# Optimization experiments

Measured on AMD Instinct MI355X. Metric: run time of the kernel, lower is better.

The kernel has to match this reference:

```python
import jax, jax.numpy as jnp
import numpy as np
from jax import lax

# Per-tensor power-of-two scales (ScalingImplType.CONST / POWER_OF_TWO in Brevitas)
S_ACT8 = 2.0 ** -4   # 8-bit signed input quant scale
S_ACT4 = 2.0 ** -1   # 4-bit signed input quant scale
S_W = 2.0 ** -2      # per-tensor weight quant scale
S_RELU = 2.0 ** -2   # 4-bit unsigned QuantReLU scale


def fq(x, scale, qmin, qmax):
    # fake-quant with straight-through estimator (STE)
    q = jnp.clip(jnp.round(x / scale), qmin, qmax) * scale
    return x + lax.stop_gradient(q - x)


def fq_signed(x, scale, bits):
    return fq(x, scale, -(2 ** (bits - 1)), 2 ** (bits - 1) - 1)


def fq_uint(x, scale, bits):
    return fq(x, scale, 0, 2 ** bits - 1)


def qconv(x, w, in_bits, w_bits, s_in, stride=1, padding=0, groups=1):
    xq = fq_signed(x, s_in, in_bits)
    wq = fq_signed(w, S_W, w_bits)
    return lax.conv_general_dilated(
        xq, wq, (stride, stride), [(padding, padding)] * 2,
        feature_group_count=groups,
        dimension_numbers=('NCHW', 'OIHW', 'NCHW'))


def maxpool(x, k, s):
    return lax.reduce_window(x, -jnp.inf, lax.max,
                             (1, 1, k, k), (1, 1, s, s), 'VALID')


def dwsep(x, dw, pw):
    c = x.shape[1]
    x = qconv(x, dw, 4, 4, S_ACT4, padding=1, groups=c)  # depthwise 3x3
    x = qconv(x, pw, 4, 4, S_ACT4)                       # pointwise 1x1
    return x


def qrelu4(x):
    return fq_uint(jax.nn.relu(x), S_RELU, 4)


def setup_inputs() -> dict:
    key = jax.random.key(0)
    ks = jax.random.split(key, 10)
    B = 1024
    mk = lambda k, shp, sc=0.5: jax.random.normal(k, shp, jnp.float32) * sc
    return {
        'x': jax.random.normal(ks[0], (B, 3, 32, 32), jnp.float32),
        'w0': mk(ks[1], (3, 3, 1, 1)),
        'dw1': mk(ks[2], (3, 1, 3, 3)),
        'pw1': mk(ks[3], (32, 3, 1, 1)),
        'dw2': mk(ks[4], (32, 1, 3, 3)),
        'pw2': mk(ks[5], (64, 32, 1, 1)),
        'dw3': mk(ks[6], (64, 1, 3, 3)),
        'pw3': mk(ks[7], (128, 64, 1, 1)),
        'wc1': mk(ks[8], (256, 128, 1, 1)),
        'wc2': mk(ks[9], (10, 256, 1, 1)),
    }


def reference(x, w0, dw1, pw1, dw2, pw2, dw3, pw3, wc1, wc2):
    # features
    h = qconv(x, w0, 8, 8, S_ACT8)            # 1x1, 3->3, 8-bit
    h = dwsep(h, dw1, pw1)                    # 3->32, 32x32
    h = qrelu4(h)
    h = maxpool(h, 2, 2)                      # 16x16
    h = dwsep(h, dw2, pw2)                    # 32->64
    h = qrelu4(h)
    h = maxpool(h, 2, 2)                      # 8x8
    h = dwsep(h, dw3, pw3)                    # 64->128
    h = qrelu4(h)
    h = maxpool(h, 8, 1)                      # 1x1
    # classifier
    h = qconv(h, wc1, 4, 4, S_ACT4)           # 128->256
    h = qrelu4(h)
    h = qconv(h, wc2, 4, 4, S_ACT4)           # 256->10
    h = fq_signed(h, S_ACT8, 8)               # output quant int8
    return h
```

## Files before the change

kernel.cpp:

```cpp
#include <hip/hip_runtime.h>

typedef int v4i __attribute__((ext_vector_type(4)));

#define W0i   0
#define DW1i  9
#define PW1i  36
#define DW2i  132
#define WC1p  3556
#define WC2p  11748
#define PW2Fb 12388
#define PW3Fb 12900
#define DW2pk 14948
#define DW3pk 15092
#define WTOT  15380

__device__ __forceinline__ int iclamp(int v, int lo, int hi) {
  return v < lo ? lo : (v > hi ? hi : v);
}
__device__ __forceinline__ int rne4(int a) {
  return (a + 1 + ((a >> 2) & 1)) >> 2;
}
__device__ __forceinline__ int rne32(int a) {
  return (a + 15 + ((a >> 5) & 1)) >> 5;
}

__device__ __forceinline__ void bar_lds() {
  asm volatile("s_waitcnt lgkmcnt(0)\n\ts_barrier" ::: "memory");
}

__device__ __forceinline__ int dot4(int a, int b, int c) {
#if defined(__has_builtin) && __has_builtin(__builtin_amdgcn_sdot4)
  return __builtin_amdgcn_sdot4(a, b, c, false);
#else
  c += ((a << 24) >> 24) * ((b << 24) >> 24);
  c += ((a << 16) >> 24) * ((b << 16) >> 24);
  c += ((a <<  8) >> 24) * ((b <<  8) >> 24);
  c += (a >> 24) * (b >> 24);
  return c;
#endif
}

__device__ __forceinline__ int alignb(int hi, int lo, int sh) {
#if defined(__has_builtin) && __has_builtin(__builtin_amdgcn_alignbyte)
  return __builtin_amdgcn_alignbyte(hi, lo, sh);
#else
  return (int)(((((unsigned long long)(unsigned)hi) << 32) |
                (unsigned)lo) >> (8 * sh));
#endif
}

__device__ __forceinline__ int pack3(int a, int b, int c) {
  return (a & 0xff) | ((b & 0xff) << 8) | ((c & 0xff) << 16);
}

__device__ __forceinline__ int pk_mad16(int a, int b, int c) {
  int d;
  asm("v_pk_mad_i16 %0, %1, %2, %3" : "=v"(d) : "v"(a), "v"(b), "v"(c));
  return d;
}
__device__ __forceinline__ int pk_add16(int a, int b) {
  int d;
  asm("v_pk_add_i16 %0, %1, %2" : "=v"(d) : "v"(a), "v"(b));
  return d;
}
__device__ __forceinline__ int pk_ashr16(int sh, int a) {
  int d;
  asm("v_pk_ashrrev_i16 %0, %1, %2" : "=v"(d) : "v"(sh), "v"(a));
  return d;
}
__device__ __forceinline__ int pk_max16(int a, int b) {
  int d;
  asm("v_pk_max_i16 %0, %1, %2" : "=v"(d) : "v"(a), "v"(b));
  return d;
}
__device__ __forceinline__ int pk_min16(int a, int b) {
  int d;
  asm("v_pk_min_i16 %0, %1, %2" : "=v"(d) : "v"(a), "v"(b));
  return d;
}
__device__ __forceinline__ int rne4s_pk(int a) {
  const int sh = 0x00020002, one = 0x00010001;
  int t = pk_ashr16(sh, a);
  t &= one;
  t += one;
  int s4 = pk_add16(a, t);
  int r = pk_ashr16(sh, s4);
  r = pk_max16(r, (int)0xFFF8FFF8);
  r = pk_min16(r, 0x00070007);
  return r;
}

__device__ __forceinline__ int max4(v4i d) {
  int a = d[0] > d[1] ? d[0] : d[1];
  int b = d[2] > d[3] ? d[2] : d[3];
  return a > b ? a : b;
}

__global__ __launch_bounds__(256) void prep_weights(
    const float* __restrict__ w0,  const float* __restrict__ dw1,
    const float* __restrict__ pw1, const float* __restrict__ dw2,
    const float* __restrict__ pw2, const float* __restrict__ dw3,
    const float* __restrict__ pw3, const float* __restrict__ wc1,
    const float* __restrict__ wc2, int* __restrict__ ws) {
  int t = blockIdx.x * blockDim.x + threadIdx.x;
  if (t >= WTOT) return;
  if (t >= DW2i && t < WC1p) return;
  if (t < DW2i) {
    float w; int lo = -8, hi = 7;
    if (t < DW1i)      { w = w0[t];        lo = -128; hi = 127; }
    else if (t < PW1i)   w = dw1[t - DW1i];
    else                 w = pw1[t - PW1i];
    ws[t] = iclamp((int)rintf(w * 4.f), lo, hi);
  } else if (t < PW2Fb) {
    const float* src = (t < WC2p) ? wc1 + (t - WC1p) * 4
                                  : wc2 + (t - WC2p) * 4;
    int p = 0;
#pragma unroll
    for (int b = 0; b < 4; b++) {
      int c = iclamp((int)rintf(src[b] * 4.f), -8, 7);
      p |= (c & 0xff) << (8 * b);
    }
    ws[t] = p;
  } else if (t < PW3Fb) {
    int i = t - PW2Fb;
    int nt = i >> 7, r = i & 127, lane = r >> 1, dw = r & 1;
    int n = nt * 16 + (lane & 15);
    int kb = (lane >> 4) * 8 + dw * 4;
    int p = 0;
#pragma unroll
    for (int b = 0; b < 4; b++) {
      int c = iclamp((int)rintf(pw2[n * 32 + kb + b] * 4.f), -8, 7);
      p |= (c & 0xff) << (8 * b);
    }
    ws[t] = p;
  } else if (t < DW2pk) {
    int i = t - PW3Fb;
    int g = i >> 7, r = i & 127, lane = r >> 1, dw = r & 1;
    int nt = g >> 1, kh = g & 1;
    int n = nt * 16 + (lane & 15);
    int kb = kh * 32 + (lane >> 4) * 8 + dw * 4;
    int p = 0;
#pragma unroll
    for (int b = 0; b < 4; b++) {
      int c = iclamp((int)rintf(pw3[n * 64 + kb + b] * 4.f), -8, 7);
      p |= (c & 0xff) << (8 * b);
    }
    ws[t] = p;
  } else if (t < DW3pk) {
    int i = t - DW2pk;
    int cq = i / 18, r = i - cq * 18, t9 = r >> 1, par = r & 1;
    int wl = iclamp((int)rintf(dw2[(cq * 4 + par) * 9 + t9] * 4.f), -8, 7);
    int wh = iclamp((int)rintf(dw2[(cq * 4 + 2 + par) * 9 + t9] * 4.f), -8, 7);
    ws[t] = (wl & 0xFFFF) | (wh << 16);
  } else {
    int i = t - DW3pk;
    int cq = i / 18, r = i - cq * 18, t9 = r >> 1, par = r & 1;
    int wl = iclamp((int)rintf(dw3[(cq * 4 + par) * 9 + t9] * 4.f), -8, 7);
    int wh = iclamp((int)rintf(dw3[(cq * 4 + 2 + par) * 9 + t9] * 4.f), -8, 7);
    ws[t] = (wl & 0xFFFF) | (wh << 16);
  }
}

__global__ __launch_bounds__(256, 4) void fused_net(
    const float* __restrict__ x,
    const int*   __restrict__ wq,
    float* __restrict__ out)
{
  const int img = blockIdx.x;
  const int tid = threadIdx.x;
  const int wv = tid >> 6, lane = tid & 63;
  const int lm = lane & 15, kg = lane >> 4;

  __shared__ __align__(16) int bufAi[2560];
  __shared__ __align__(16) int bufBi[2592];

  const int ntp = (wv & 1) * 2;
  const long bw0 = *(const long*)(wq + PW2Fb + (ntp * 64 + lane) * 2);
  const long bw1 = *(const long*)(wq + PW2Fb + ((ntp + 1) * 64 + lane) * 2);
  long b0v[2], b1v[2];
#pragma unroll
  for (int h = 0; h < 2; h++) {
    int nt = wv * 2 + h;
    b0v[h] = *(const long*)(wq + PW3Fb + (nt * 2 + 0) * 128 + lane * 2);
    b1v[h] = *(const long*)(wq + PW3Fb + (nt * 2 + 1) * 128 + lane * 2);
  }

  {
    const float* xim = x + (size_t)img * 3072;
    const int p4 = tid * 4;
    float4 v0 = *(const float4*)(xim + p4);
    float4 v1 = *(const float4*)(xim + 1024 + p4);
    float4 v2 = *(const float4*)(xim + 2048 + p4);
    int w[9];
#pragma unroll
    for (int i = 0; i < 9; i++) w[i] = wq[W0i + i];
#define Q8(v) iclamp((int)rintf((v) * 16.f), -128, 127)
    int a0[4] = {Q8(v0.x), Q8(v0.y), Q8(v0.z), Q8(v0.w)};
    int a1[4] = {Q8(v1.x), Q8(v1.y), Q8(v1.z), Q8(v1.w)};
    int a2[4] = {Q8(v2.x), Q8(v2.y), Q8(v2.z), Q8(v2.w)};
#undef Q8
#pragma unroll
    for (int o = 0; o < 3; o++) {
      int pk = 0;
#pragma unroll
      for (int j = 0; j < 4; j++) {
        int s = a0[j] * w[o * 3] + a1[j] * w[o * 3 + 1] + a2[j] * w[o * 3 + 2];
        pk |= (iclamp(rne32(s), -8, 7) & 0xff) << (8 * j);
      }
      bufAi[o * 256 + tid] = pk;
    }
  }
  bar_lds();

  {
    const int py = tid >> 4, px = tid & 15;
    int wr[3][3], wrh[3][3];
#pragma unroll
    for (int c = 0; c < 3; c++)
#pragma unroll
      for (int ky = 0; ky < 3; ky++) {
        int w = pack3(wq[DW1i + c * 9 + ky * 3],
                      wq[DW1i + c * 9 + ky * 3 + 1],
                      wq[DW1i + c * 9 + ky * 3 + 2]);
        wr[c][ky] = w;
        wrh[c][ky] = w << 8;
      }
    const int s = (px & 1) ? 1 : 3;
    const int D0 = (2 * px - 1) >> 2;
    int V[3][4];
#pragma unroll
    for (int r = 0; r < 4; r++) {
      int rr = 2 * py - 1 + r;
      bool ok = (unsigned)rr < 32u;
#pragma unroll
      for (int c = 0; c < 3; c++) {
        int lo = 0, hi = 0;
        if (ok) {
          const int* ap = bufAi + c * 256 + rr * 8;
          if (px > 0)  lo = ap[D0];
          if (px < 15) hi = ap[D0 + 1];
        }
        V[c][r] = alignb(hi, lo, s);
      }
    }
    int a[4];
#pragma unroll
    for (int dy = 0; dy < 2; dy++) {
      int r01[3];
#pragma unroll
      for (int c = 0; c < 3; c++) {
        int acc0 = 0, acc1 = 0;
#pragma unroll
        for (int ky = 0; ky < 3; ky++) {
          acc0 = dot4(V[c][dy + ky], wr[c][ky], acc0);
          acc1 = dot4(V[c][dy + ky], wrh[c][ky], acc1);
        }
        int p = (int)__builtin_amdgcn_perm((unsigned)acc1, (unsigned)acc0,
                                           0x05040100u);
        r01[c] = rne4s_pk(p);
      }
      unsigned t0 = __builtin_amdgcn_perm((unsigned)r01[1], (unsigned)r01[0],
                                          0x0C0C0400u);
      a[2 * dy] = (int)__builtin_amdgcn_perm((unsigned)r01[2], t0, 0x0C040100u);
      unsigned t1 = __builtin_amdgcn_perm((unsigned)r01[1], (unsigned)r01[0],
                                          0x0C0C0602u);
      a[2 * dy + 1] =
          (int)__builtin_amdgcn_perm((unsigned)r01[2], t1, 0x0C060100u);
    }
#pragma unroll
    for (int it = 0; it < 8; it++) {
      int pk = 0;
#pragma unroll
      for (int j = 0; j < 4; j++) {
        int o = it * 4 + j;
        int wpk = pack3(wq[PW1i + o * 3], wq[PW1i + o * 3 + 1],
                        wq[PW1i + o * 3 + 2]);
        int m0 = dot4(a[0], wpk, 0), m1 = dot4(a[1], wpk, 0);
        int m2 = dot4(a[2], wpk, 0), m3 = dot4(a[3], wpk, 0);
        int mx = max(max(m0, m1), max(m2, m3));
        pk |= iclamp(rne4(mx), 0, 7) << (8 * j);
      }
      bufBi[py * 149 + px * 9 + it] = pk;
    }
  }
  bar_lds();

  {
    const int cq = tid >> 5;
    const int rem = tid & 31;
    const int y = rem >> 1, xh = rem & 1, x0 = xh * 8;
    int we[9], wo[9];
    {
      const int2* wp = (const int2*)(wq + DW2pk + cq * 18);
#pragma unroll
      for (int t9 = 0; t9 < 9; t9++) { int2 v = wp[t9]; we[t9] = v.x; wo[t9] = v.y; }
    }
    int acce[8] = {}, acco[8] = {};
#pragma unroll
    for (int ky = 0; ky < 3; ky++) {
      int yy = y + ky - 1;
      if (yy < 0 || yy > 15) continue;
      int rb = yy * 149 + cq;
      int rd[10];
      rd[0] = (x0 > 0) ? bufBi[rb + (x0 - 1) * 9] : 0;
#pragma unroll
      for (int k = 1; k < 9; k++) rd[k] = bufBi[rb + (x0 - 1 + k) * 9];
      rd[9] = (x0 < 8) ? bufBi[rb + (x0 + 8) * 9] : 0;
      int ee[10], eo[10];
#pragma unroll
      for (int k = 0; k < 10; k++) {
        ee[k] = rd[k] & 0x000F000F;
        eo[k] = (rd[k] >> 8) & 0x000F000F;
      }
#pragma unroll
      for (int j = 0; j < 8; j++)
#pragma unroll
        for (int kx = 0; kx < 3; kx++) {
          acce[j] = pk_mad16(ee[j + kx], we[ky * 3 + kx], acce[j]);
          acco[j] = pk_mad16(eo[j + kx], wo[ky * 3 + kx], acco[j]);
        }
    }
    const int py = y >> 1, dy = y & 1;
#pragma unroll
    for (int j = 0; j < 8; j++) {
      int xx = x0 + j;
      int qp = py * 8 + (xx >> 1);
      int q = qp ^ (py & 3);
      int m = q * 4 + dy * 2 + (xx & 1);
      int re = rne4s_pk(acce[j]);
      int ro = rne4s_pk(acco[j]);
      bufAi[m * 10 + cq] = (re & 0x00FF00FF) | ((ro & 0x00FF00FF) << 8);
    }
  }
  bar_lds();

  {
    const int mtb = (wv >> 1) * 8;
    const signed char* Ab = (const signed char*)bufAi;
    signed char* A2c = (signed char*)bufBi;
    const int n0 = ntp * 16 + lm, n1 = (ntp + 1) * 16 + lm;
#pragma unroll 4
    for (int mt = mtb; mt < mtb + 8; mt++) {
      int m = mt * 16 + lm;
      long av = *(const long*)(Ab + m * 40 + kg * 8);
      v4i d0 = __builtin_amdgcn_mfma_i32_16x16x32_i8(av, bw0, (v4i){0, 0, 0, 0},
                                                     0, 0, 0);
      v4i d1 = __builtin_amdgcn_mfma_i32_16x16x32_i8(av, bw1, (v4i){0, 0, 0, 0},
                                                     0, 0, 0);
      int q = mt * 4 + kg;
      int qp = q ^ ((q >> 3) & 3);
      int py = qp >> 3, px = qp & 7;
      int bb = (py * 137 + px * 17) * 4;
      A2c[bb + n0] = (signed char)iclamp(rne4(max4(d0)), 0, 7);
      A2c[bb + n1] = (signed char)iclamp(rne4(max4(d1)), 0, 7);
    }
  }
  bar_lds();

  {
    int cq2 = tid >> 4;
    int s = tid & 15;
    int y = s >> 1, x0 = (s & 1) << 2;
    int we[9], wo[9];
    {
      const int2* wp = (const int2*)(wq + DW3pk + cq2 * 18);
#pragma unroll
      for (int t9 = 0; t9 < 9; t9++) { int2 v = wp[t9]; we[t9] = v.x; wo[t9] = v.y; }
    }
    int acce[4] = {}, acco[4] = {};
#pragma unroll
    for (int ky = 0; ky < 3; ky++) {
      int yy = y + ky - 1;
      if (yy < 0 || yy > 7) continue;
      int rb = yy * 137 + cq2;
      int rd[6];
      rd[0] = (x0 == 4) ? bufBi[rb + (x0 - 1) * 17] : 0;
      rd[1] = bufBi[rb + x0 * 17];
      rd[2] = bufBi[rb + (x0 + 1) * 17];
      rd[3] = bufBi[rb + (x0 + 2) * 17];
      rd[4] = bufBi[rb + (x0 + 3) * 17];
      rd[5] = (x0 == 0) ? bufBi[rb + (x0 + 4) * 17] : 0;
      int ee[6], eo[6];
#pragma unroll
      for (int k = 0; k < 6; k++) {
        ee[k] = rd[k] & 0x000F000F;
        eo[k] = (rd[k] >> 8) & 0x000F000F;
      }
#pragma unroll
      for (int j = 0; j < 4; j++)
#pragma unroll
        for (int kx = 0; kx < 3; kx++) {
          acce[j] = pk_mad16(ee[j + kx], we[ky * 3 + kx], acce[j]);
          acco[j] = pk_mad16(eo[j + kx], wo[ky * 3 + kx], acco[j]);
        }
    }
#pragma unroll
    for (int j = 0; j < 4; j++) {
      int re = rne4s_pk(acce[j]);
      int ro = rne4s_pk(acco[j]);
      bufAi[(y * 8 + x0 + j) * 18 + cq2] =
          (re & 0x00FF00FF) | ((ro & 0x00FF00FF) << 8);
    }
  }
  int4 wfc[8];
  {
    const int4* wp = (const int4*)(wq + WC1p + tid * 32);
#pragma unroll
    for (int rI = 0; rI < 8; rI++) wfc[rI] = wp[rI];
  }
  bar_lds();

  {
    const signed char* Ab = (const signed char*)bufAi;
    signed char* fcin = (signed char*)bufBi;
    int mx[2] = {-1000000, -1000000};
#pragma unroll
    for (int mt = 0; mt < 4; mt++) {
      int m = mt * 16 + lm;
      long a0 = *(const long*)(Ab + m * 72 + kg * 8);
      long a1 = *(const long*)(Ab + m * 72 + 32 + kg * 8);
#pragma unroll
      for (int h = 0; h < 2; h++) {
        v4i d = __builtin_amdgcn_mfma_i32_16x16x32_i8(a0, b0v[h],
                                                      (v4i){0, 0, 0, 0}, 0, 0, 0);
        d = __builtin_amdgcn_mfma_i32_16x16x32_i8(a1, b1v[h], d, 0, 0, 0);
        int t4 = max4(d);
        mx[h] = mx[h] > t4 ? mx[h] : t4;
      }
    }
#pragma unroll
    for (int h = 0; h < 2; h++) {
      int red = max(mx[h], __shfl_xor(mx[h], 16));
      red = max(red, __shfl_xor(red, 32));
      if (lane < 16)
        fcin[(wv * 2 + h) * 16 + lm] = (signed char)iclamp(rne4(red), 0, 7);
    }
  }
  bar_lds();

  {
    const int4* mp = (const int4*)bufBi;
    int acc = 0;
#pragma unroll
    for (int rI = 0; rI < 8; rI++) {
      int4 a = mp[rI]; int4 w = wfc[rI];
      acc = dot4(a.x, w.x, acc); acc = dot4(a.y, w.y, acc);
      acc = dot4(a.z, w.z, acc); acc = dot4(a.w, w.w, acc);
    }
    ((signed char*)bufAi)[tid] = (signed char)iclamp(rne4(acc), 0, 7);
  }
  bar_lds();

  if (tid < 40) {
    int k = tid >> 2, j = tid & 3;
    const int4* wp = (const int4*)(wq + WC2p + k * 64 + j * 16);
    const int4* ap = (const int4*)bufAi;
    int acc = 0;
#pragma unroll
    for (int r = 0; r < 4; r++) {
      int4 a = ap[j * 4 + r]; int4 w = wp[r];
      acc = dot4(a.x, w.x, acc); acc = dot4(a.y, w.y, acc);
      acc = dot4(a.z, w.z, acc); acc = dot4(a.w, w.w, acc);
    }
    acc += __shfl_xor(acc, 1);
    acc += __shfl_xor(acc, 2);
    if (j == 0) {
      int code = iclamp(2 * acc, -128, 127);
      out[(size_t)img * 10 + k] = (float)code * 0.0625f;
    }
  }
}

extern "C" void kernel_launch(void* const* d_in, const int* in_sizes, int n_in,
                              void* d_out, int out_size, void* d_ws, size_t ws_size,
                              hipStream_t stream) {
  const float* x   = (const float*)d_in[0];
  const float* w0  = (const float*)d_in[1];
  const float* dw1 = (const float*)d_in[2];
  const float* pw1 = (const float*)d_in[3];
  const float* dw2 = (const float*)d_in[4];
  const float* pw2 = (const float*)d_in[5];
  const float* dw3 = (const float*)d_in[6];
  const float* pw3 = (const float*)d_in[7];
  const float* wc1 = (const float*)d_in[8];
  const float* wc2 = (const float*)d_in[9];
  int*   wsq = (int*)d_ws;
  float* out = (float*)d_out;

  prep_weights<<<(WTOT + 255) / 256, 256, 0, stream>>>(
      w0, dw1, pw1, dw2, pw2, dw3, pw3, wc1, wc2, wsq);
  fused_net<<<1024, 256, 0, stream>>>(x, wsq, out);
}
```

Before: 93.06 us.

## Fold weight quantization into fused kernel and drop separate prep launch

Removes the prep_weights kernel and has every block quantize and pack the weights itself, straight from the float inputs. Small depthwise and pointwise weights are staged into shared memory, and MFMA and classifier weights are quantized in registers. This removes one kernel launch and the dependency between the two kernels. In exchange, each of the 1024 blocks re-reads the float weights, including 128 KB of wc1, and repeats the quantization arithmetic, which adds redundant global traffic and ALU work.

Measured after the change: 115.4 us. +24.1%, slower.

```diff
diff --git a/kernel.cpp b/kernel.cpp
--- a/kernel.cpp
+++ b/kernel.cpp
@@ -2,17 +2,12 @@
 
 typedef int v4i __attribute__((ext_vector_type(4)));
 
-#define W0i   0
-#define DW1i  9
-#define PW1i  36
-#define DW2i  132
-#define WC1p  3556
-#define WC2p  11748
-#define PW2Fb 12388
-#define PW3Fb 12900
-#define DW2pk 14948
-#define DW3pk 15092
-#define WTOT  15380
+#define W0s   0
+#define DW1s  9
+#define DW2s  18
+#define DW3s  162
+#define PW1s  452
+#define WSMN  484
 
 __device__ __forceinline__ int iclamp(int v, int lo, int hi) {
   return v < lo ? lo : (v > hi ? hi : v);
@@ -53,6 +48,20 @@
   return (a & 0xff) | ((b & 0xff) << 8) | ((c & 0xff) << 16);
 }
 
+__device__ __forceinline__ int q4w(float w) {
+  return iclamp((int)rintf(w * 4.f), -8, 7);
+}
+__device__ __forceinline__ int qpack4(const float* p) {
+  float4 v = *(const float4*)p;
+  return (q4w(v.x) & 0xff) | ((q4w(v.y) & 0xff) << 8) |
+         ((q4w(v.z) & 0xff) << 16) | (q4w(v.w) << 24);
+}
+__device__ __forceinline__ long qpack8(const float* p) {
+  unsigned lo = (unsigned)qpack4(p);
+  unsigned hi = (unsigned)qpack4(p + 4);
+  return (long)(((unsigned long long)hi << 32) | lo);
+}
+
 __device__ __forceinline__ int pk_mad16(int a, int b, int c) {
   int d;
   asm("v_pk_mad_i16 %0, %1, %2, %3" : "=v"(d) : "v"(a), "v"(b), "v"(c));
@@ -96,74 +105,13 @@
   return a > b ? a : b;
 }
 
-__global__ __launch_bounds__(256) void prep_weights(
-    const float* __restrict__ w0,  const float* __restrict__ dw1,
-    const float* __restrict__ pw1, const float* __restrict__ dw2,
-    const float* __restrict__ pw2, const float* __restrict__ dw3,
-    const float* __restrict__ pw3, const float* __restrict__ wc1,
-    const float* __restrict__ wc2, int* __restrict__ ws) {
-  int t = blockIdx.x * blockDim.x + threadIdx.x;
-  if (t >= WTOT) return;
-  if (t >= DW2i && t < WC1p) return;
-  if (t < DW2i) {
-    float w; int lo = -8, hi = 7;
-    if (t < DW1i)      { w = w0[t];        lo = -128; hi = 127; }
-    else if (t < PW1i)   w = dw1[t - DW1i];
-    else                 w = pw1[t - PW1i];
-    ws[t] = iclamp((int)rintf(w * 4.f), lo, hi);
-  } else if (t < PW2Fb) {
-    const float* src = (t < WC2p) ? wc1 + (t - WC1p) * 4
-                                  : wc2 + (t - WC2p) * 4;
-    int p = 0;
-#pragma unroll
-    for (int b = 0; b < 4; b++) {
-      int c = iclamp((int)rintf(src[b] * 4.f), -8, 7);
-      p |= (c & 0xff) << (8 * b);
-    }
-    ws[t] = p;
-  } else if (t < PW3Fb) {
-    int i = t - PW2Fb;
-    int nt = i >> 7, r = i & 127, lane = r >> 1, dw = r & 1;
-    int n = nt * 16 + (lane & 15);
-    int kb = (lane >> 4) * 8 + dw * 4;
-    int p = 0;
-#pragma unroll
-    for (int b = 0; b < 4; b++) {
-      int c = iclamp((int)rintf(pw2[n * 32 + kb + b] * 4.f), -8, 7);
-      p |= (c & 0xff) << (8 * b);
-    }
-    ws[t] = p;
-  } else if (t < DW2pk) {
-    int i = t - PW3Fb;
-    int g = i >> 7, r = i & 127, lane = r >> 1, dw = r & 1;
-    int nt = g >> 1, kh = g & 1;
-    int n = nt * 16 + (lane & 15);
-    int kb = kh * 32 + (lane >> 4) * 8 + dw * 4;
-    int p = 0;
-#pragma unroll
-    for (int b = 0; b < 4; b++) {
-      int c = iclamp((int)rintf(pw3[n * 64 + kb + b] * 4.f), -8, 7);
-      p |= (c & 0xff) << (8 * b);
-    }
-    ws[t] = p;
-  } else if (t < DW3pk) {
-    int i = t - DW2pk;
-    int cq = i / 18, r = i - cq * 18, t9 = r >> 1, par = r & 1;
-    int wl = iclamp((int)rintf(dw2[(cq * 4 + par) * 9 + t9] * 4.f), -8, 7);
-    int wh = iclamp((int)rintf(dw2[(cq * 4 + 2 + par) * 9 + t9] * 4.f), -8, 7);
-    ws[t] = (wl & 0xFFFF) | (wh << 16);
-  } else {
-    int i = t - DW3pk;
-    int cq = i / 18, r = i - cq * 18, t9 = r >> 1, par = r & 1;
-    int wl = iclamp((int)rintf(dw3[(cq * 4 + par) * 9 + t9] * 4.f), -8, 7);
-    int wh = iclamp((int)rintf(dw3[(cq * 4 + 2 + par) * 9 + t9] * 4.f), -8, 7);
-    ws[t] = (wl & 0xFFFF) | (wh << 16);
-  }
-}
-
 __global__ __launch_bounds__(256, 4) void fused_net(
     const float* __restrict__ x,
-    const int*   __restrict__ wq,
+    const float* __restrict__ w0f,  const float* __restrict__ dw1f,
+    const float* __restrict__ pw1f, const float* __restrict__ dw2f,
+    const float* __restrict__ pw2f, const float* __restrict__ dw3f,
+    const float* __restrict__ pw3f, const float* __restrict__ wc1f,
+    const float* __restrict__ wc2f,
     float* __restrict__ out)
 {
   const int img = blockIdx.x;
@@ -173,38 +121,73 @@
 
   __shared__ __align__(16) int bufAi[2560];
   __shared__ __align__(16) int bufBi[2592];
+  __shared__ __align__(16) int wsm[WSMN];
 
   const int ntp = (wv & 1) * 2;
-  const long bw0 = *(const long*)(wq + PW2Fb + (ntp * 64 + lane) * 2);
-  const long bw1 = *(const long*)(wq + PW2Fb + ((ntp + 1) * 64 + lane) * 2);
-  long b0v[2], b1v[2];
-#pragma unroll
-  for (int h = 0; h < 2; h++) {
-    int nt = wv * 2 + h;
-    b0v[h] = *(const long*)(wq + PW3Fb + (nt * 2 + 0) * 128 + lane * 2);
-    b1v[h] = *(const long*)(wq + PW3Fb + (nt * 2 + 1) * 128 + lane * 2);
-  }
-
-  {
-    const float* xim = x + (size_t)img * 3072;
-    const int p4 = tid * 4;
-    float4 v0 = *(const float4*)(xim + p4);
-    float4 v1 = *(const float4*)(xim + 1024 + p4);
-    float4 v2 = *(const float4*)(xim + 2048 + p4);
+  long bw0, bw1, b0v[2], b1v[2];
+  {
+    const int n0 = ntp * 16 + lm, n1 = (ntp + 1) * 16 + lm;
+    bw0 = qpack8(pw2f + n0 * 32 + kg * 8);
+    bw1 = qpack8(pw2f + n1 * 32 + kg * 8);
+#pragma unroll
+    for (int h = 0; h < 2; h++) {
+      int n = (wv * 2 + h) * 16 + lm;
+      b0v[h] = qpack8(pw3f + n * 64 + kg * 8);
+      b1v[h] = qpack8(pw3f + n * 64 + 32 + kg * 8);
+    }
+  }
+
+  for (int t = tid; t < WSMN; t += 256) {
+    int v;
+    if (t < 9) {
+      v = iclamp((int)rintf(w0f[t] * 4.f), -128, 127);
+    } else if (t < 18) {
+      int i = (t - 9) * 3;
+      v = pack3(q4w(dw1f[i]), q4w(dw1f[i + 1]), q4w(dw1f[i + 2]));
+    } else if (t < 162) {
+      int i = t - DW2s;
+      int cq = i / 18, r = i - cq * 18, t9 = r >> 1, par = r & 1;
+      int wl = q4w(dw2f[(cq * 4 + par) * 9 + t9]);
+      int wh = q4w(dw2f[(cq * 4 + 2 + par) * 9 + t9]);
+      v = (wl & 0xFFFF) | (wh << 16);
+    } else if (t < 450) {
+      int i = t - DW3s;
+      int cq = i / 18, r = i - cq * 18, t9 = r >> 1, par = r & 1;
+      int wl = q4w(dw3f[(cq * 4 + par) * 9 + t9]);
+      int wh = q4w(dw3f[(cq * 4 + 2 + par) * 9 + t9]);
+      v = (wl & 0xFFFF) | (wh << 16);
+    } else if (t >= PW1s) {
+      int o = (t - PW1s) * 3;
+      v = pack3(q4w(pw1f[o]), q4w(pw1f[o + 1]), q4w(pw1f[o + 2]));
+    } else {
+      continue;
+    }
+    wsm[t] = v;
+  }
+
+  const float* xim = x + (size_t)img * 3072;
+  const int p4 = tid * 4;
+  float4 v0 = *(const float4*)(xim + p4);
+  float4 v1 = *(const float4*)(xim + 1024 + p4);
+  float4 v2 = *(const float4*)(xim + 2048 + p4);
+#define Q8(v) iclamp((int)rintf((v) * 16.f), -128, 127)
+  int a0q[4] = {Q8(v0.x), Q8(v0.y), Q8(v0.z), Q8(v0.w)};
+  int a1q[4] = {Q8(v1.x), Q8(v1.y), Q8(v1.z), Q8(v1.w)};
+  int a2q[4] = {Q8(v2.x), Q8(v2.y), Q8(v2.z), Q8(v2.w)};
+#undef Q8
+  bar_lds();
+
+  {
     int w[9];
 #pragma unroll
-    for (int i = 0; i < 9; i++) w[i] = wq[W0i + i];
-#define Q8(v) iclamp((int)rintf((v) * 16.f), -128, 127)
-    int a0[4] = {Q8(v0.x), Q8(v0.y), Q8(v0.z), Q8(v0.w)};
-    int a1[4] = {Q8(v1.x), Q8(v1.y), Q8(v1.z), Q8(v1.w)};
-    int a2[4] = {Q8(v2.x), Q8(v2.y), Q8(v2.z), Q8(v2.w)};
-#undef Q8
+    for (int i = 0; i < 9; i++) w[i] = wsm[W0s + i];
 #pragma unroll
     for (int o = 0; o < 3; o++) {
       int pk = 0;
 #pragma unroll
       for (int j = 0; j < 4; j++) {
-        int s = a0[j] * w[o * 3] + a1[j] * w[o * 3 + 1] + a2[j] * w[o * 3 + 2];
+        int s = a0q[j] * w[o * 3] + a1q[j] * w[o * 3 + 1] +
+                a2q[j] * w[o * 3 + 2];
         pk |= (iclamp(rne32(s), -8, 7) & 0xff) << (8 * j);
       }
       bufAi[o * 256 + tid] = pk;
@@ -219,9 +202,7 @@
     for (int c = 0; c < 3; c++)
 #pragma unroll
       for (int ky = 0; ky < 3; ky++) {
-        int w = pack3(wq[DW1i + c * 9 + ky * 3],
-                      wq[DW1i + c * 9 + ky * 3 + 1],
-                      wq[DW1i + c * 9 + ky * 3 + 2]);
+        int w = wsm[DW1s + c * 3 + ky];
         wr[c][ky] = w;
         wrh[c][ky] = w << 8;
       }
@@ -273,8 +254,7 @@
 #pragma unroll
       for (int j = 0; j < 4; j++) {
         int o = it * 4 + j;
-        int wpk = pack3(wq[PW1i + o * 3], wq[PW1i + o * 3 + 1],
-                        wq[PW1i + o * 3 + 2]);
+        int wpk = wsm[PW1s + o];
         int m0 = dot4(a[0], wpk, 0), m1 = dot4(a[1], wpk, 0);
         int m2 = dot4(a[2], wpk, 0), m3 = dot4(a[3], wpk, 0);
         int mx = max(max(m0, m1), max(m2, m3));
@@ -291,7 +271,7 @@
     const int y = rem >> 1, xh = rem & 1, x0 = xh * 8;
     int we[9], wo[9];
     {
-      const int2* wp = (const int2*)(wq + DW2pk + cq * 18);
+      const int2* wp = (const int2*)(wsm + DW2s + cq * 18);
 #pragma unroll
       for (int t9 = 0; t9 < 9; t9++) { int2 v = wp[t9]; we[t9] = v.x; wo[t9] = v.y; }
     }
@@ -363,7 +343,7 @@
     int y = s >> 1, x0 = (s & 1) << 2;
     int we[9], wo[9];
     {
-      const int2* wp = (const int2*)(wq + DW3pk + cq2 * 18);
+      const int2* wp = (const int2*)(wsm + DW3s + cq2 * 18);
 #pragma unroll
       for (int t9 = 0; t9 < 9; t9++) { int2 v = wp[t9]; we[t9] = v.x; wo[t9] = v.y; }
     }
@@ -404,9 +384,16 @@
   }
   int4 wfc[8];
   {
-    const int4* wp = (const int4*)(wq + WC1p + tid * 32);
-#pragma unroll
-    for (int rI = 0; rI < 8; rI++) wfc[rI] = wp[rI];
+    const float* wp = wc1f + (size_t)tid * 128;
+#pragma unroll 2
+    for (int rI = 0; rI < 8; rI++) {
+      int4 w;
+      w.x = qpack4(wp + rI * 16);
+      w.y = qpack4(wp + rI * 16 + 4);
+      w.z = qpack4(wp + rI * 16 + 8);
+      w.w = qpack4(wp + rI * 16 + 12);
+      wfc[rI] = w;
+    }
   }
   bar_lds();
 
@@ -453,14 +440,17 @@
 
   if (tid < 40) {
     int k = tid >> 2, j = tid & 3;
-    const int4* wp = (const int4*)(wq + WC2p + k * 64 + j * 16);
+    const float* wp = wc2f + k * 256 + j * 64;
     const int4* ap = (const int4*)bufAi;
     int acc = 0;
 #pragma unroll
     for (int r = 0; r < 4; r++) {
-      int4 a = ap[j * 4 + r]; int4 w = wp[r];
-      acc = dot4(a.x, w.x, acc); acc = dot4(a.y, w.y, acc);
-      acc = dot4(a.z, w.z, acc); acc = dot4(a.w, w.w, acc);
+      const float* wr4 = wp + r * 16;
+      int4 a = ap[j * 4 + r];
+      acc = dot4(a.x, qpack4(wr4), acc);
+      acc = dot4(a.y, qpack4(wr4 + 4), acc);
+      acc = dot4(a.z, qpack4(wr4 + 8), acc);
+      acc = dot4(a.w, qpack4(wr4 + 12), acc);
     }
     acc += __shfl_xor(acc, 1);
     acc += __shfl_xor(acc, 2);
@@ -474,20 +464,10 @@
 extern "C" void kernel_launch(void* const* d_in, const int* in_sizes, int n_in,
                               void* d_out, int out_size, void* d_ws, size_t ws_size,
                               hipStream_t stream) {
-  const float* x   = (const float*)d_in[0];
-  const float* w0  = (const float*)d_in[1];
-  const float* dw1 = (const float*)d_in[2];
-  const float* pw1 = (const float*)d_in[3];
-  const float* dw2 = (const float*)d_in[4];
-  const float* pw2 = (const float*)d_in[5];
-  const float* dw3 = (const float*)d_in[6];
-  const float* pw3 = (const float*)d_in[7];
-  const float* wc1 = (const float*)d_in[8];
-  const float* wc2 = (const float*)d_in[9];
-  int*   wsq = (int*)d_ws;
-  float* out = (float*)d_out;
-
-  prep_weights<<<(WTOT + 255) / 256, 256, 0, stream>>>(
-      w0, dw1, pw1, dw2, pw2, dw3, pw3, wc1, wc2, wsq);
-  fused_net<<<1024, 256, 0, stream>>>(x, wsq, out);
-}
+  (void)d_ws; (void)ws_size; (void)in_sizes; (void)n_in; (void)out_size;
+  fused_net<<<1024, 256, 0, stream>>>(
+      (const float*)d_in[0], (const float*)d_in[1], (const float*)d_in[2],
+      (const float*)d_in[3], (const float*)d_in[4], (const float*)d_in[5],
+      (const float*)d_in[6], (const float*)d_in[7], (const float*)d_in[8],
+      (const float*)d_in[9], (float*)d_out);
+}
```
